# Optimization experiments

Hardware: AMD Instinct MI355X
Metric: run time of the kernel (lower is better)

## Reference

```python
import jax, jax.numpy as jnp
import numpy as np

B, N, K = 2, 50000, 16
CIN, COUT, M = 64, 32, 4


def setup_inputs() -> dict:
    key = jax.random.key(0)
    ks = jax.random.split(key, 7)
    x = jax.random.normal(ks[0], (B, N, CIN), dtype=jnp.float32)
    adj = jax.random.randint(ks[1], (B, N, K), 0, N + 1)  # 0 == empty slot
    weight = jax.random.normal(ks[2], (M, COUT, CIN), dtype=jnp.float32) * 0.1
    bias = jax.random.normal(ks[3], (COUT,), dtype=jnp.float32) * 0.1
    u = jax.random.normal(ks[4], (M, CIN), dtype=jnp.float32) * 0.1
    v = jax.random.normal(ks[5], (M, CIN), dtype=jnp.float32) * 0.1
    c = jax.random.normal(ks[6], (M,), dtype=jnp.float32) * 0.1
    return {"x": x, "adj": adj, "weight": weight, "bias": bias,
            "u": u, "v": v, "c": c}


def _gather_padded(feat, adj):
    # feat: (B, N, ...); adj: (B, N, K) indices into zero-padded node axis
    # (index 0 selects the zero row, matching torch get_patches semantics)
    pad = jnp.zeros((feat.shape[0], 1) + feat.shape[2:], feat.dtype)
    feat_p = jnp.concatenate([pad, feat], axis=1)        # (B, N+1, ...)
    return jax.vmap(lambda f, a: f[a])(feat_p, adj)      # (B, N, K, ...)


def reference(x, adj, weight, bias, u, v, c):
    # degree normalization: 1/#nonzero-neighbors, 0 for isolated points
    deg = jnp.sum(adj != 0, axis=-1).astype(x.dtype)     # (B, N)
    inv_deg = jnp.where(deg != 0, 1.0 / deg, 0.0)        # (B, N)

    # mixture-kernel transform of every node, then neighbor gather
    wx = jnp.einsum('bnc,moc->bnmo', x, weight)          # (B, N, M, COUT)
    gathered = _gather_padded(wx, adj)                   # (B, N, K, M, COUT)

    # softmax-gated assignment q[b,n,k,m] = softmax_m(v.x_nbr + u.x_ctr + c)
    ux = jnp.einsum('mc,bnc->bnm', u, x)                 # (B, N, M)
    vx = jnp.einsum('mc,bnc->bnm', v, x)                 # (B, N, M)
    vg = _gather_padded(vx, adj)                         # (B, N, K, M)
    q = jax.nn.softmax(vg + ux[:, :, None, :] + c, axis=-1)

    # weighted sum over neighbors K and mixture components M
    out = jnp.einsum('bnkm,bnkmo->bno', q, gathered)     # (B, N, COUT)
    return out * inv_deg[..., None] + bias
```

## Files before the change

kernel.cpp:

```cpp
#include <hip/hip_runtime.h>

namespace {
constexpr int BB = 2;
constexpr int NN = 50000;
constexpr int KK = 16;
constexpr int CI = 64;
constexpr int CO = 32;
constexpr int MM = 4;
constexpr int BN = BB * NN;
constexpr int GROUPS = NN / 4;
constexpr int GRID = 1024;
constexpr int WAVES = (GRID / 2) * 4;
}

typedef __attribute__((ext_vector_type(8))) short short8v;
typedef __attribute__((ext_vector_type(4))) float float4v;

__device__ __forceinline__ unsigned short bf16r(float f) {
  unsigned int u = __float_as_uint(f);
  u += 0x7FFFu + ((u >> 16) & 1u);
  return (unsigned short)(u >> 16);
}

__global__ __launch_bounds__(256) void k_prep(
    const float* __restrict__ x, const float* __restrict__ u,
    const float* __restrict__ v, float* __restrict__ ux,
    float* __restrict__ vx, unsigned short* __restrict__ xh) {
  int idx = blockIdx.x * 256 + threadIdx.x;
  if (idx >= BN) return;
  const float4* xr = (const float4*)(x + (size_t)idx * CI);
  float su[MM] = {0.f, 0.f, 0.f, 0.f};
  float sv[MM] = {0.f, 0.f, 0.f, 0.f};
  uint4 xpack[8];
#pragma unroll
  for (int t = 0; t < CI / 4; ++t) {
    float4 xv = xr[t];
#pragma unroll
    for (int m = 0; m < MM; ++m) {
      float4 uv = *(const float4*)(u + m * CI + t * 4);
      float4 vv = *(const float4*)(v + m * CI + t * 4);
      su[m] += uv.x * xv.x + uv.y * xv.y + uv.z * xv.z + uv.w * xv.w;
      sv[m] += vv.x * xv.x + vv.y * xv.y + vv.z * xv.z + vv.w * xv.w;
    }
    unsigned d0 = (unsigned)bf16r(xv.x) | ((unsigned)bf16r(xv.y) << 16);
    unsigned d1 = (unsigned)bf16r(xv.z) | ((unsigned)bf16r(xv.w) << 16);
    if (t & 1) {
      xpack[t >> 1].z = d0;
      xpack[t >> 1].w = d1;
    } else {
      xpack[t >> 1].x = d0;
      xpack[t >> 1].y = d1;
    }
  }
  ((float4*)ux)[idx] = make_float4(su[0], su[1], su[2], su[3]);
  ((float4*)vx)[idx] = make_float4(sv[0], sv[1], sv[2], sv[3]);
  uint4* xo = (uint4*)(xh + (size_t)idx * CI);
#pragma unroll
  for (int t = 0; t < 8; ++t) xo[t] = xpack[t];
}

__global__ __launch_bounds__(256, 4) void k_gather(
    const unsigned short* __restrict__ xh, const int* __restrict__ adj,
    const float* __restrict__ weight, const float* __restrict__ bias,
    const float* __restrict__ cvec, const float* __restrict__ ux,
    const float* __restrict__ vx, float* __restrict__ out) {
  __shared__ unsigned short w_lds[2 * 8 * 64 * 8];
  __shared__ unsigned short t_lds[4][8 * 256];
  __shared__ float q_lds[4][4][64];
  __shared__ float inv_lds[4][8];

  const int tid = threadIdx.x;
  const int lane = tid & 63;
  const int wv = tid >> 6;

  for (int i = tid; i < 2 * 8 * 64; i += 256) {
    int tl = i >> 9;
    int ks = (i >> 6) & 7;
    int l = i & 63;
    int o = tl * 16 + (l & 15);
    unsigned pk[4];
#pragma unroll
    for (int ee = 0; ee < 4; ++ee) {
      int k0 = ks * 32 + (l >> 4) * 8 + 2 * ee;
      unsigned lo = bf16r(weight[((k0 & 3) * CO + o) * CI + (k0 >> 2)]);
      unsigned hi =
          bf16r(weight[(((k0 + 1) & 3) * CO + o) * CI + ((k0 + 1) >> 2)]);
      pk[ee] = lo | (hi << 16);
    }
    *(uint4*)&w_lds[i * 8] = make_uint4(pk[0], pk[1], pk[2], pk[3]);
  }
  __syncthreads();

  const int m4 = lane & 3;
  const int k4 = lane >> 2;
  const float cm = cvec[m4];
  const float b0 = bias[lane & 15];
  const float b1 = bias[16 + (lane & 15)];

  const int xcd = blockIdx.x & 7;
  const int b = xcd >> 2;
  const int wb = ((blockIdx.x >> 3) << 2) | (xcd & 3);
  const int w = wb * 4 + wv;
  const size_t bbase = (size_t)b * NN;
  const unsigned short* xhb = xh + bbase * CI;
  const float* vxb = vx + bbase * MM;
  unsigned short* twv = t_lds[wv];

  int g = w;
  int av = 0;
  if (g < GROUPS) av = adj[(bbase + (size_t)g * 4) * KK + lane];
  int jrows = 0;
  int gbase = g;

#define LOADS(n, GV)                                                       \
  _Pragma("unroll") for (int k = 0; k < KK; ++k) {                         \
    int r = __builtin_amdgcn_readlane(av_c, (n)*16 + k);                   \
    const unsigned short* rp = xhb + (size_t)(max(r, 1) - 1) * CI;         \
    GV[k] = rp[lane];                                                      \
  }

#define ACC_NODE(n, GV)                                                    \
  {                                                                        \
    const float4* qp = (const float4*)&q_lds[wv][n][0];                    \
    float t0 = 0.f, t1 = 0.f, t2 = 0.f, t3 = 0.f;                          \
    _Pragma("unroll") for (int k = 0; k < KK; ++k) {                       \
      float xv = __uint_as_float(GV[k] << 16);                             \
      float4 qv = qp[k];                                                   \
      t0 = fmaf(qv.x, xv, t0);                                             \
      t1 = fmaf(qv.y, xv, t1);                                             \
      t2 = fmaf(qv.z, xv, t2);                                             \
      t3 = fmaf(qv.w, xv, t3);                                             \
    }                                                                      \
    unsigned lo = (unsigned)bf16r(t0) | ((unsigned)bf16r(t1) << 16);       \
    unsigned hi = (unsigned)bf16r(t2) | ((unsigned)bf16r(t3) << 16);       \
    int row = jrows * 4 + (n);                                             \
    unsigned boff =                                                        \
        (unsigned)row * 512u + (((unsigned)lane * 8u) ^                    \
                                ((unsigned)(row & 7) << 4));               \
    *(uint2*)((char*)twv + boff) = make_uint2(lo, hi);                     \
  }

#define FLUSH(JC)                                                          \
  {                                                                        \
    float4v ac0 = {0.f, 0.f, 0.f, 0.f};                                    \
    float4v ac1 = {0.f, 0.f, 0.f, 0.f};                                    \
    const int arow = lane & 7;                                             \
    const unsigned axor = (unsigned)(arow & 7) << 4;                       \
    _Pragma("unroll") for (int ks = 0; ks < 8; ++ks) {                     \
      unsigned aoff =                                                      \
          (unsigned)arow * 512u +                                          \
          ((((unsigned)(lane >> 4)) * 16u + (unsigned)ks * 64u) ^ axor);   \
      short8v A = *(const short8v*)((const char*)twv + aoff);              \
      short8v Bl = *(const short8v*)&w_lds[(0 * 8 + ks) * 512 + lane * 8]; \
      short8v Bh = *(const short8v*)&w_lds[(1 * 8 + ks) * 512 + lane * 8]; \
      ac0 = __builtin_amdgcn_mfma_f32_16x16x32_bf16(A, Bl, ac0, 0, 0, 0);  \
      ac1 = __builtin_amdgcn_mfma_f32_16x16x32_bf16(A, Bh, ac1, 0, 0, 0);  \
    }                                                                      \
    int jj = lane >> 4;                                                    \
    int gg = gbase + jj * WAVES;                                           \
    if (jj < (JC) && gg < GROUPS) {                                        \
      float4 iv = *(const float4*)&inv_lds[wv][jj * 4];                    \
      float* op = out + (bbase + (size_t)gg * 4) * CO + (lane & 15);       \
      op[0] = ac0[0] * iv.x + b0;                                          \
      op[16] = ac1[0] * iv.x + b1;                                         \
      op[32] = ac0[1] * iv.y + b0;                                         \
      op[48] = ac1[1] * iv.y + b1;                                         \
      op[64] = ac0[2] * iv.z + b0;                                         \
      op[80] = ac1[2] * iv.z + b1;                                         \
      op[96] = ac0[3] * iv.w + b0;                                         \
      op[112] = ac1[3] * iv.w + b1;                                        \
    }                                                                      \
  }

  while (g < GROUPS) {
    const int av_c = av;
    const size_t bn0 = bbase + (size_t)g * 4;

    int as0 = __shfl(av_c, k4);
    int as1 = __shfl(av_c, 16 + k4);
    int as2 = __shfl(av_c, 32 + k4);
    int as3 = __shfl(av_c, 48 + k4);
    float vg0 = vxb[(size_t)(max(as0, 1) - 1) * MM + m4];
    float vg1 = vxb[(size_t)(max(as1, 1) - 1) * MM + m4];
    float vg2 = vxb[(size_t)(max(as2, 1) - 1) * MM + m4];
    float vg3 = vxb[(size_t)(max(as3, 1) - 1) * MM + m4];
    float ux0 = ux[bn0 * MM + m4];
    float ux1 = ux[(bn0 + 1) * MM + m4];
    float ux2 = ux[(bn0 + 2) * MM + m4];
    float ux3 = ux[(bn0 + 3) * MM + m4];
    const unsigned long long msk = __ballot(av_c != 0);

    unsigned gv0[KK], gv1[KK], gv2[KK], gv3[KK];
    LOADS(0, gv0)
    LOADS(1, gv1)

    const int gn = g + WAVES;
    if (gn < GROUPS) av = adj[(bbase + (size_t)gn * 4) * KK + lane];

    float i0, i1, i2, i3;
    {
      int d0 = __popc((unsigned)(msk & 0xFFFFull));
      int d1 = __popc((unsigned)((msk >> 16) & 0xFFFFull));
      int d2 = __popc((unsigned)((msk >> 32) & 0xFFFFull));
      int d3 = __popc((unsigned)((msk >> 48) & 0xFFFFull));
      i0 = d0 ? __builtin_amdgcn_rcpf((float)d0) : 0.f;
      i1 = d1 ? __builtin_amdgcn_rcpf((float)d1) : 0.f;
      i2 = d2 ? __builtin_amdgcn_rcpf((float)d2) : 0.f;
      i3 = d3 ? __builtin_amdgcn_rcpf((float)d3) : 0.f;
      float e0 = __expf(vg0 + ux0 + cm);
      float e1 = __expf(vg1 + ux1 + cm);
      float e2 = __expf(vg2 + ux2 + cm);
      float e3 = __expf(vg3 + ux3 + cm);
      float s0 = e0 + __shfl_xor(e0, 1);
      float s1 = e1 + __shfl_xor(e1, 1);
      float s2 = e2 + __shfl_xor(e2, 1);
      float s3 = e3 + __shfl_xor(e3, 1);
      s0 += __shfl_xor(s0, 2);
      s1 += __shfl_xor(s1, 2);
      s2 += __shfl_xor(s2, 2);
      s3 += __shfl_xor(s3, 2);
      q_lds[wv][0][lane] = (as0 != 0) ? e0 * __builtin_amdgcn_rcpf(s0) : 0.f;
      q_lds[wv][1][lane] = (as1 != 0) ? e1 * __builtin_amdgcn_rcpf(s1) : 0.f;
      q_lds[wv][2][lane] = (as2 != 0) ? e2 * __builtin_amdgcn_rcpf(s2) : 0.f;
      q_lds[wv][3][lane] = (as3 != 0) ? e3 * __builtin_amdgcn_rcpf(s3) : 0.f;
      if (lane == 0)
        *(float4*)&inv_lds[wv][jrows * 4] = make_float4(i0, i1, i2, i3);
    }

    ACC_NODE(0, gv0)
    LOADS(2, gv2)
    ACC_NODE(1, gv1)
    LOADS(3, gv3)
    ACC_NODE(2, gv2)
    ACC_NODE(3, gv3)

    ++jrows;
    g = gn;
    if (jrows == 2) {
      FLUSH(2)
      jrows = 0;
      gbase = g;
    }
  }
  if (jrows > 0) FLUSH(jrows)
}

__global__ __launch_bounds__(256) void k_uxvx(
    const float* __restrict__ x, const float* __restrict__ u,
    const float* __restrict__ v, float* __restrict__ ux,
    float* __restrict__ vx) {
  int idx = blockIdx.x * 256 + threadIdx.x;
  if (idx >= BN) return;
  const float4* xr = (const float4*)(x + (size_t)idx * CI);
  float su[MM] = {0.f, 0.f, 0.f, 0.f};
  float sv[MM] = {0.f, 0.f, 0.f, 0.f};
#pragma unroll
  for (int t = 0; t < CI / 4; ++t) {
    float4 xv = xr[t];
#pragma unroll
    for (int m = 0; m < MM; ++m) {
      float4 uv = *(const float4*)(u + m * CI + t * 4);
      float4 vv = *(const float4*)(v + m * CI + t * 4);
      su[m] += uv.x * xv.x + uv.y * xv.y + uv.z * xv.z + uv.w * xv.w;
      sv[m] += vv.x * xv.x + vv.y * xv.y + vv.z * xv.z + vv.w * xv.w;
    }
  }
  ((float4*)ux)[idx] = make_float4(su[0], su[1], su[2], su[3]);
  ((float4*)vx)[idx] = make_float4(sv[0], sv[1], sv[2], sv[3]);
}

__global__ __launch_bounds__(256) void k_main_old(
    const float* __restrict__ x, const int* __restrict__ adj,
    const float* __restrict__ weight, const float* __restrict__ bias,
    const float* __restrict__ cvec, const float* __restrict__ ux,
    const float* __restrict__ vx, float* __restrict__ out) {
  __shared__ float w_lds[MM][CO][CI + 4];
  __shared__ float q_lds2[4][64];
  __shared__ float t_lds2[4][MM][CI];
  const int tid = threadIdx.x;
  const int lane = tid & 63;
  const int wv = tid >> 6;
#pragma unroll
  for (int i = 0; i < (MM * CO * CI) / 256; ++i) {
    int g = i * 256 + tid;
    w_lds[g >> 11][(g >> 6) & (CO - 1)][g & (CI - 1)] = weight[g];
  }
  __syncthreads();
  const int k4 = lane >> 2;
  const int m4 = lane & 3;
  const int o = lane & 31;
  const int hh = lane >> 5;
  const float cm = cvec[m4];
  const float bo = bias[o];
  for (int g = blockIdx.x; g < BN / 4; g += gridDim.x) {
    const int bn = g * 4 + wv;
    const int b = (bn >= NN) ? 1 : 0;
    const int* adjp = adj + (size_t)bn * KK;
    const float* xb = x + (size_t)b * NN * CI;
    int4 A[4];
#pragma unroll
    for (int i = 0; i < 4; ++i) A[i] = ((const int4*)adjp)[i];
    int deg = 0;
#pragma unroll
    for (int i = 0; i < 4; ++i)
      deg += (A[i].x != 0) + (A[i].y != 0) + (A[i].z != 0) + (A[i].w != 0);
    const float inv_deg = (deg > 0) ? 1.0f / (float)deg : 0.0f;
    int a = adjp[k4];
    float vg = 0.f;
    if (a != 0) vg = vx[((size_t)b * NN + (a - 1)) * MM + m4];
    float logit = vg + ux[(size_t)bn * MM + m4] + cm;
    float mx = fmaxf(logit, __shfl_xor(logit, 1));
    mx = fmaxf(mx, __shfl_xor(mx, 2));
    float e = __expf(logit - mx);
    float s = e + __shfl_xor(e, 1);
    s += __shfl_xor(s, 2);
    q_lds2[wv][lane] = (a != 0) ? (e / s) : 0.f;
    int rows[KK];
    {
      int tmp[KK] = {A[0].x, A[0].y, A[0].z, A[0].w, A[1].x, A[1].y,
                     A[1].z, A[1].w, A[2].x, A[2].y, A[2].z, A[2].w,
                     A[3].x, A[3].y, A[3].z, A[3].w};
#pragma unroll
      for (int k = 0; k < KK; ++k) rows[k] = max(tmp[k], 1) - 1;
    }
    float xg[KK];
#pragma unroll
    for (int k = 0; k < KK; ++k) xg[k] = xb[(size_t)rows[k] * CI + lane];
    float t0 = 0.f, t1 = 0.f, t2 = 0.f, t3 = 0.f;
#pragma unroll
    for (int k = 0; k < KK; ++k) {
      float4 qv = *(const float4*)&q_lds2[wv][k * 4];
      t0 += qv.x * xg[k];
      t1 += qv.y * xg[k];
      t2 += qv.z * xg[k];
      t3 += qv.w * xg[k];
    }
    t_lds2[wv][0][lane] = t0;
    t_lds2[wv][1][lane] = t1;
    t_lds2[wv][2][lane] = t2;
    t_lds2[wv][3][lane] = t3;
    float a0 = 0.f, a1 = 0.f, a2 = 0.f, a3 = 0.f;
#pragma unroll
    for (int mm = 0; mm < 2; ++mm) {
      const float* wrow = &w_lds[2 * hh + mm][o][0];
      const float* trow = &t_lds2[wv][2 * hh + mm][0];
#pragma unroll
      for (int t4 = 0; t4 < CI / 4; ++t4) {
        float4 wvv = *(const float4*)(wrow + 4 * t4);
        float4 tv = *(const float4*)(trow + 4 * t4);
        a0 += wvv.x * tv.x;
        a1 += wvv.y * tv.y;
        a2 += wvv.z * tv.z;
        a3 += wvv.w * tv.w;
      }
    }
    float acc = (a0 + a1) + (a2 + a3);
    acc += __shfl_xor(acc, 32);
    if (lane < 32) out[(size_t)bn * CO + o] = acc * inv_deg + bo;
  }
}

extern "C" void kernel_launch(void* const* d_in, const int* in_sizes, int n_in,
                              void* d_out, int out_size, void* d_ws,
                              size_t ws_size, hipStream_t stream) {
  const float* x = (const float*)d_in[0];
  const int* adj = (const int*)d_in[1];
  const float* weight = (const float*)d_in[2];
  const float* bias = (const float*)d_in[3];
  const float* u = (const float*)d_in[4];
  const float* v = (const float*)d_in[5];
  const float* cvec = (const float*)d_in[6];
  float* out = (float*)d_out;

  float* ux = (float*)d_ws;
  float* vx = ux + (size_t)BN * MM;
  const size_t base = (size_t)BN * MM * 2 * sizeof(float);
  const size_t need = base + (size_t)BN * CI * sizeof(unsigned short);

  if (ws_size >= need) {
    unsigned short* xhb = (unsigned short*)((char*)d_ws + base);
    k_prep<<<(BN + 255) / 256, 256, 0, stream>>>(x, u, v, ux, vx, xhb);
    k_gather<<<GRID, 256, 0, stream>>>(xhb, adj, weight, bias, cvec, ux, vx,
                                       out);
  } else {
    k_uxvx<<<(BN + 255) / 256, 256, 0, stream>>>(x, u, v, ux, vx);
    k_main_old<<<1024, 256, 0, stream>>>(x, adj, weight, bias, cvec, ux, vx,
                                         out);
  }
}
```

Measured before the change: 73.78 us.

## Split fused gather+MFMA kernel into gather-to-workspace and separate MFMA output kernel

The fused gather kernel is split in two. The first kernel computes the q-weighted neighbor sums, folds the inverse degree into q, and writes bf16 intermediate rows to a workspace buffer at higher occupancy with a larger grid. The second kernel runs the bf16 MFMA projection with the weights and adds the bias. This takes the MFMA, LDS staging and register pressure out of the latency-bound gather loop, at the cost of an extra launch and about 51 MB of intermediate writes and reads. The old fp32 fallback is removed, and without enough workspace the fused kernel runs instead.

```diff
diff --git a/kernel.cpp b/kernel.cpp
--- a/kernel.cpp
+++ b/kernel.cpp
@@ -9,8 +9,10 @@
 constexpr int MM = 4;
 constexpr int BN = BB * NN;
 constexpr int GROUPS = NN / 4;
-constexpr int GRID = 1024;
-constexpr int WAVES = (GRID / 2) * 4;
+constexpr int GRID_G = 1536;
+constexpr int WAVES_G = (GRID_G / 2) * 4;
+constexpr int GRID_MID = 1024;
+constexpr int WAVES_MID = (GRID_MID / 2) * 4;
 }
 
 typedef __attribute__((ext_vector_type(8))) short short8v;
@@ -59,7 +61,174 @@
   for (int t = 0; t < 8; ++t) xo[t] = xpack[t];
 }
 
-__global__ __launch_bounds__(256, 4) void k_gather(
+__global__ __launch_bounds__(256, 6) void k_gather2(
+    const unsigned short* __restrict__ xh, const int* __restrict__ adj,
+    const float* __restrict__ cvec, const float* __restrict__ ux,
+    const float* __restrict__ vx, unsigned short* __restrict__ th) {
+  __shared__ float q_lds[4][4][64];
+  const int tid = threadIdx.x;
+  const int lane = tid & 63;
+  const int wv = tid >> 6;
+  const int m4 = lane & 3;
+  const int k4 = lane >> 2;
+  const float cm = cvec[m4];
+
+  const int xcd = blockIdx.x & 7;
+  const int b = xcd >> 2;
+  const int wb = ((blockIdx.x >> 3) << 2) | (xcd & 3);
+  const int w = wb * 4 + wv;
+  const size_t bbase = (size_t)b * NN;
+  const unsigned short* xhb = xh + bbase * CI;
+  const float* vxb = vx + bbase * MM;
+
+  int g = w;
+  int av = 0;
+  if (g < GROUPS) av = adj[(bbase + (size_t)g * 4) * KK + lane];
+
+#define LOADS2(n, GV)                                                      \
+  _Pragma("unroll") for (int k = 0; k < KK; ++k) {                         \
+    int r = __builtin_amdgcn_readlane(av_c, (n)*16 + k);                   \
+    const unsigned short* rp = xhb + (size_t)(max(r, 1) - 1) * CI;         \
+    GV[k] = rp[lane];                                                      \
+  }
+
+#define ACC2(n, GV)                                                        \
+  {                                                                        \
+    const float4* qp = (const float4*)&q_lds[wv][n][0];                    \
+    float t0 = 0.f, t1 = 0.f, t2 = 0.f, t3 = 0.f;                          \
+    _Pragma("unroll") for (int k = 0; k < KK; ++k) {                       \
+      float xv = __uint_as_float(GV[k] << 16);                             \
+      float4 qv = qp[k];                                                   \
+      t0 = fmaf(qv.x, xv, t0);                                             \
+      t1 = fmaf(qv.y, xv, t1);                                             \
+      t2 = fmaf(qv.z, xv, t2);                                             \
+      t3 = fmaf(qv.w, xv, t3);                                             \
+    }                                                                      \
+    unsigned lo = (unsigned)bf16r(t0) | ((unsigned)bf16r(t1) << 16);       \
+    unsigned hi = (unsigned)bf16r(t2) | ((unsigned)bf16r(t3) << 16);       \
+    *(uint2*)(th + (bn0 + (n)) * 256 + lane * 4) = make_uint2(lo, hi);     \
+  }
+
+  while (g < GROUPS) {
+    const int av_c = av;
+    const size_t bn0 = bbase + (size_t)g * 4;
+
+    int as0 = __shfl(av_c, k4);
+    int as1 = __shfl(av_c, 16 + k4);
+    int as2 = __shfl(av_c, 32 + k4);
+    int as3 = __shfl(av_c, 48 + k4);
+    float vg0 = vxb[(size_t)(max(as0, 1) - 1) * MM + m4];
+    float vg1 = vxb[(size_t)(max(as1, 1) - 1) * MM + m4];
+    float vg2 = vxb[(size_t)(max(as2, 1) - 1) * MM + m4];
+    float vg3 = vxb[(size_t)(max(as3, 1) - 1) * MM + m4];
+    float ux0 = ux[bn0 * MM + m4];
+    float ux1 = ux[(bn0 + 1) * MM + m4];
+    float ux2 = ux[(bn0 + 2) * MM + m4];
+    float ux3 = ux[(bn0 + 3) * MM + m4];
+    const unsigned long long msk = __ballot(av_c != 0);
+
+    unsigned gv0[KK], gv1[KK], gv2[KK], gv3[KK];
+    LOADS2(0, gv0)
+    LOADS2(1, gv1)
+
+    const int gn = g + WAVES_G;
+    if (gn < GROUPS) av = adj[(bbase + (size_t)gn * 4) * KK + lane];
+
+    {
+      int d0 = __popc((unsigned)(msk & 0xFFFFull));
+      int d1 = __popc((unsigned)((msk >> 16) & 0xFFFFull));
+      int d2 = __popc((unsigned)((msk >> 32) & 0xFFFFull));
+      int d3 = __popc((unsigned)((msk >> 48) & 0xFFFFull));
+      float i0 = d0 ? __builtin_amdgcn_rcpf((float)d0) : 0.f;
+      float i1 = d1 ? __builtin_amdgcn_rcpf((float)d1) : 0.f;
+      float i2 = d2 ? __builtin_amdgcn_rcpf((float)d2) : 0.f;
+      float i3 = d3 ? __builtin_amdgcn_rcpf((float)d3) : 0.f;
+      float e0 = __expf(vg0 + ux0 + cm);
+      float e1 = __expf(vg1 + ux1 + cm);
+      float e2 = __expf(vg2 + ux2 + cm);
+      float e3 = __expf(vg3 + ux3 + cm);
+      float s0 = e0 + __shfl_xor(e0, 1);
+      float s1 = e1 + __shfl_xor(e1, 1);
+      float s2 = e2 + __shfl_xor(e2, 1);
+      float s3 = e3 + __shfl_xor(e3, 1);
+      s0 += __shfl_xor(s0, 2);
+      s1 += __shfl_xor(s1, 2);
+      s2 += __shfl_xor(s2, 2);
+      s3 += __shfl_xor(s3, 2);
+      q_lds[wv][0][lane] =
+          (as0 != 0) ? e0 * __builtin_amdgcn_rcpf(s0) * i0 : 0.f;
+      q_lds[wv][1][lane] =
+          (as1 != 0) ? e1 * __builtin_amdgcn_rcpf(s1) * i1 : 0.f;
+      q_lds[wv][2][lane] =
+          (as2 != 0) ? e2 * __builtin_amdgcn_rcpf(s2) * i2 : 0.f;
+      q_lds[wv][3][lane] =
+          (as3 != 0) ? e3 * __builtin_amdgcn_rcpf(s3) * i3 : 0.f;
+    }
+
+    ACC2(0, gv0)
+    LOADS2(2, gv2)
+    ACC2(1, gv1)
+    LOADS2(3, gv3)
+    ACC2(2, gv2)
+    ACC2(3, gv3)
+
+    g = gn;
+  }
+}
+
+__global__ __launch_bounds__(256) void k_out(
+    const unsigned short* __restrict__ th, const float* __restrict__ weight,
+    const float* __restrict__ bias, float* __restrict__ out) {
+  __shared__ unsigned short w_lds[2 * 8 * 64 * 8];
+  const int tid = threadIdx.x;
+  for (int i = tid; i < 2 * 8 * 64; i += 256) {
+    int tl = i >> 9;
+    int ks = (i >> 6) & 7;
+    int l = i & 63;
+    int o = tl * 16 + (l & 15);
+    unsigned pk[4];
+#pragma unroll
+    for (int ee = 0; ee < 4; ++ee) {
+      int k0 = ks * 32 + (l >> 4) * 8 + 2 * ee;
+      unsigned lo = bf16r(weight[((k0 & 3) * CO + o) * CI + (k0 >> 2)]);
+      unsigned hi =
+          bf16r(weight[(((k0 + 1) & 3) * CO + o) * CI + ((k0 + 1) >> 2)]);
+      pk[ee] = lo | (hi << 16);
+    }
+    *(uint4*)&w_lds[i * 8] = make_uint4(pk[0], pk[1], pk[2], pk[3]);
+  }
+  __syncthreads();
+
+  const int lane = tid & 63;
+  const int wv = tid >> 6;
+  const int l15 = lane & 15;
+  const int lq = lane >> 4;
+  const float bo0 = bias[l15];
+  const float bo1 = bias[16 + l15];
+  const float4v zero = {0.f, 0.f, 0.f, 0.f};
+
+  for (int t = blockIdx.x * 4 + wv; t < BN / 16; t += gridDim.x * 4) {
+    const int n0 = t * 16;
+    const unsigned short* tp = th + (size_t)(n0 + l15) * 256 + lq * 8;
+    float4v ac0 = zero, ac1 = zero;
+#pragma unroll
+    for (int ks = 0; ks < 8; ++ks) {
+      short8v A = *(const short8v*)(tp + ks * 32);
+      short8v Bl = *(const short8v*)&w_lds[(0 * 8 + ks) * 512 + lane * 8];
+      short8v Bh = *(const short8v*)&w_lds[(1 * 8 + ks) * 512 + lane * 8];
+      ac0 = __builtin_amdgcn_mfma_f32_16x16x32_bf16(A, Bl, ac0, 0, 0, 0);
+      ac1 = __builtin_amdgcn_mfma_f32_16x16x32_bf16(A, Bh, ac1, 0, 0, 0);
+    }
+#pragma unroll
+    for (int ri = 0; ri < 4; ++ri) {
+      size_t node = (size_t)(n0 + lq * 4 + ri);
+      out[node * CO + l15] = ac0[ri] + bo0;
+      out[node * CO + 16 + l15] = ac1[ri] + bo1;
+    }
+  }
+}
+
+__global__ __launch_bounds__(256, 4) void k_gather_mid(
     const unsigned short* __restrict__ xh, const int* __restrict__ adj,
     const float* __restrict__ weight, const float* __restrict__ bias,
     const float* __restrict__ cvec, const float* __restrict__ ux,
@@ -134,9 +303,8 @@
     unsigned lo = (unsigned)bf16r(t0) | ((unsigned)bf16r(t1) << 16);       \
     unsigned hi = (unsigned)bf16r(t2) | ((unsigned)bf16r(t3) << 16);       \
     int row = jrows * 4 + (n);                                             \
-    unsigned boff =                                                        \
-        (unsigned)row * 512u + (((unsigned)lane * 8u) ^                    \
-                                ((unsigned)(row & 7) << 4));               \
+    unsigned boff = (unsigned)row * 512u +                                 \
+                    (((unsigned)lane * 8u) ^ ((unsigned)(row & 7) << 4));  \
     *(uint2*)((char*)twv + boff) = make_uint2(lo, hi);                     \
   }
 
@@ -157,7 +325,7 @@
       ac1 = __builtin_amdgcn_mfma_f32_16x16x32_bf16(A, Bh, ac1, 0, 0, 0);  \
     }                                                                      \
     int jj = lane >> 4;                                                    \
-    int gg = gbase + jj * WAVES;                                           \
+    int gg = gbase + jj * WAVES_MID;                                       \
     if (jj < (JC) && gg < GROUPS) {                                        \
       float4 iv = *(const float4*)&inv_lds[wv][jj * 4];                    \
       float* op = out + (bbase + (size_t)gg * 4) * CO + (lane & 15);       \
@@ -194,7 +362,7 @@
     LOADS(0, gv0)
     LOADS(1, gv1)
 
-    const int gn = g + WAVES;
+    const int gn = g + WAVES_MID;
     if (gn < GROUPS) av = adj[(bbase + (size_t)gn * 4) * KK + lane];
 
     float i0, i1, i2, i3;
@@ -245,121 +413,6 @@
   if (jrows > 0) FLUSH(jrows)
 }
 
-__global__ __launch_bounds__(256) void k_uxvx(
-    const float* __restrict__ x, const float* __restrict__ u,
-    const float* __restrict__ v, float* __restrict__ ux,
-    float* __restrict__ vx) {
-  int idx = blockIdx.x * 256 + threadIdx.x;
-  if (idx >= BN) return;
-  const float4* xr = (const float4*)(x + (size_t)idx * CI);
-  float su[MM] = {0.f, 0.f, 0.f, 0.f};
-  float sv[MM] = {0.f, 0.f, 0.f, 0.f};
-#pragma unroll
-  for (int t = 0; t < CI / 4; ++t) {
-    float4 xv = xr[t];
-#pragma unroll
-    for (int m = 0; m < MM; ++m) {
-      float4 uv = *(const float4*)(u + m * CI + t * 4);
-      float4 vv = *(const float4*)(v + m * CI + t * 4);
-      su[m] += uv.x * xv.x + uv.y * xv.y + uv.z * xv.z + uv.w * xv.w;
-      sv[m] += vv.x * xv.x + vv.y * xv.y + vv.z * xv.z + vv.w * xv.w;
-    }
-  }
-  ((float4*)ux)[idx] = make_float4(su[0], su[1], su[2], su[3]);
-  ((float4*)vx)[idx] = make_float4(sv[0], sv[1], sv[2], sv[3]);
-}
-
-__global__ __launch_bounds__(256) void k_main_old(
-    const float* __restrict__ x, const int* __restrict__ adj,
-    const float* __restrict__ weight, const float* __restrict__ bias,
-    const float* __restrict__ cvec, const float* __restrict__ ux,
-    const float* __restrict__ vx, float* __restrict__ out) {
-  __shared__ float w_lds[MM][CO][CI + 4];
-  __shared__ float q_lds2[4][64];
-  __shared__ float t_lds2[4][MM][CI];
-  const int tid = threadIdx.x;
-  const int lane = tid & 63;
-  const int wv = tid >> 6;
-#pragma unroll
-  for (int i = 0; i < (MM * CO * CI) / 256; ++i) {
-    int g = i * 256 + tid;
-    w_lds[g >> 11][(g >> 6) & (CO - 1)][g & (CI - 1)] = weight[g];
-  }
-  __syncthreads();
-  const int k4 = lane >> 2;
-  const int m4 = lane & 3;
-  const int o = lane & 31;
-  const int hh = lane >> 5;
-  const float cm = cvec[m4];
-  const float bo = bias[o];
-  for (int g = blockIdx.x; g < BN / 4; g += gridDim.x) {
-    const int bn = g * 4 + wv;
-    const int b = (bn >= NN) ? 1 : 0;
-    const int* adjp = adj + (size_t)bn * KK;
-    const float* xb = x + (size_t)b * NN * CI;
-    int4 A[4];
-#pragma unroll
-    for (int i = 0; i < 4; ++i) A[i] = ((const int4*)adjp)[i];
-    int deg = 0;
-#pragma unroll
-    for (int i = 0; i < 4; ++i)
-      deg += (A[i].x != 0) + (A[i].y != 0) + (A[i].z != 0) + (A[i].w != 0);
-    const float inv_deg = (deg > 0) ? 1.0f / (float)deg : 0.0f;
-    int a = adjp[k4];
-    float vg = 0.f;
-    if (a != 0) vg = vx[((size_t)b * NN + (a - 1)) * MM + m4];
-    float logit = vg + ux[(size_t)bn * MM + m4] + cm;
-    float mx = fmaxf(logit, __shfl_xor(logit, 1));
-    mx = fmaxf(mx, __shfl_xor(mx, 2));
-    float e = __expf(logit - mx);
-    float s = e + __shfl_xor(e, 1);
-    s += __shfl_xor(s, 2);
-    q_lds2[wv][lane] = (a != 0) ? (e / s) : 0.f;
-    int rows[KK];
-    {
-      int tmp[KK] = {A[0].x, A[0].y, A[0].z, A[0].w, A[1].x, A[1].y,
-                     A[1].z, A[1].w, A[2].x, A[2].y, A[2].z, A[2].w,
-                     A[3].x, A[3].y, A[3].z, A[3].w};
-#pragma unroll
-      for (int k = 0; k < KK; ++k) rows[k] = max(tmp[k], 1) - 1;
-    }
-    float xg[KK];
-#pragma unroll
-    for (int k = 0; k < KK; ++k) xg[k] = xb[(size_t)rows[k] * CI + lane];
-    float t0 = 0.f, t1 = 0.f, t2 = 0.f, t3 = 0.f;
-#pragma unroll
-    for (int k = 0; k < KK; ++k) {
-      float4 qv = *(const float4*)&q_lds2[wv][k * 4];
-      t0 += qv.x * xg[k];
-      t1 += qv.y * xg[k];
-      t2 += qv.z * xg[k];
-      t3 += qv.w * xg[k];
-    }
-    t_lds2[wv][0][lane] = t0;
-    t_lds2[wv][1][lane] = t1;
-    t_lds2[wv][2][lane] = t2;
-    t_lds2[wv][3][lane] = t3;
-    float a0 = 0.f, a1 = 0.f, a2 = 0.f, a3 = 0.f;
-#pragma unroll
-    for (int mm = 0; mm < 2; ++mm) {
-      const float* wrow = &w_lds[2 * hh + mm][o][0];
-      const float* trow = &t_lds2[wv][2 * hh + mm][0];
-#pragma unroll
-      for (int t4 = 0; t4 < CI / 4; ++t4) {
-        float4 wvv = *(const float4*)(wrow + 4 * t4);
-        float4 tv = *(const float4*)(trow + 4 * t4);
-        a0 += wvv.x * tv.x;
-        a1 += wvv.y * tv.y;
-        a2 += wvv.z * tv.z;
-        a3 += wvv.w * tv.w;
-      }
-    }
-    float acc = (a0 + a1) + (a2 + a3);
-    acc += __shfl_xor(acc, 32);
-    if (lane < 32) out[(size_t)bn * CO + o] = acc * inv_deg + bo;
-  }
-}
-
 extern "C" void kernel_launch(void* const* d_in, const int* in_sizes, int n_in,
                               void* d_out, int out_size, void* d_ws,
                               size_t ws_size, hipStream_t stream) {
@@ -375,16 +428,17 @@
   float* ux = (float*)d_ws;
   float* vx = ux + (size_t)BN * MM;
   const size_t base = (size_t)BN * MM * 2 * sizeof(float);
-  const size_t need = base + (size_t)BN * CI * sizeof(unsigned short);
-
-  if (ws_size >= need) {
-    unsigned short* xhb = (unsigned short*)((char*)d_ws + base);
-    k_prep<<<(BN + 255) / 256, 256, 0, stream>>>(x, u, v, ux, vx, xhb);
-    k_gather<<<GRID, 256, 0, stream>>>(xhb, adj, weight, bias, cvec, ux, vx,
-                                       out);
+  const size_t xh_bytes = (size_t)BN * CI * sizeof(unsigned short);
+  const size_t th_bytes = (size_t)BN * 256 * sizeof(unsigned short);
+  unsigned short* xhb = (unsigned short*)((char*)d_ws + base);
+  unsigned short* thb = (unsigned short*)((char*)d_ws + base + xh_bytes);
+
+  k_prep<<<(BN + 255) / 256, 256, 0, stream>>>(x, u, v, ux, vx, xhb);
+  if (ws_size >= base + xh_bytes + th_bytes) {
+    k_gather2<<<GRID_G, 256, 0, stream>>>(xhb, adj, cvec, ux, vx, thb);
+    k_out<<<512, 256, 0, stream>>>(thb, weight, bias, out);
   } else {
-    k_uxvx<<<(BN + 255) / 256, 256, 0, stream>>>(x, u, v, ux, vx);
-    k_main_old<<<1024, 256, 0, stream>>>(x, adj, weight, bias, cvec, ux, vx,
-                                         out);
-  }
-}
+    k_gather_mid<<<GRID_MID, 256, 0, stream>>>(xhb, adj, weight, bias, cvec,
+                                               ux, vx, out);
+  }
+}
```

Result: slower. 81.92 us (+11.0%).
